# Kernel tuning notes

Measured on AMD Instinct MI355X. Metric: run time of the kernel, lower is better.

## Reference

```python
import jax, jax.numpy as jnp
import numpy as np

DT_MIN = 0.001  # config.rsp_dt_min
HARMONIC_SCALE = 0.1


def phi(z):
    # ResonantActivation: SiLU plus small harmonic term (harmonic_scale=0.1)
    return jax.nn.silu(z) + HARMONIC_SCALE * jnp.sin(z)


def setup_inputs() -> dict:
    key = jax.random.key(0)
    ks = jax.random.split(key, 8)
    B, L, D = 4, 2048, 1024
    std = 1.0 / np.sqrt(D)
    inp = {
        "x": jax.random.normal(ks[0], (B, L, D), dtype=jnp.float32),
        "f_prev": jnp.zeros((B, D), dtype=jnp.float32),
        "s_prev": jnp.zeros((B, D), dtype=jnp.float32),
        "w_lambda": jnp.zeros((D,), dtype=jnp.float32),
        "P_lambda_w": jax.random.uniform(ks[1], (D, D), jnp.float32, -std, std),
        "W_beta_w": jax.random.uniform(ks[2], (D, D), jnp.float32, -std, std),
        "W_alpha_w": jax.random.uniform(ks[3], (D, D), jnp.float32, -std, std),
        "W_alpha_b": jnp.full((D,), -3.0, dtype=jnp.float32),  # rsp_init_bias_alpha
        "W_rho_w": 0.01 * jax.random.normal(ks[4], (D, 3 * D), dtype=jnp.float32),
        "W_rho_b": jnp.full((D,), 2.0, dtype=jnp.float32),  # rsp_init_bias_rho
        "out_proj_w": 0.02 * jax.random.normal(ks[5], (D, D), dtype=jnp.float32),
        "res_scale": jnp.ones((1,), dtype=jnp.float32),
    }
    return inp


def _rsp_forward(x, f_prev, s_prev, w_lambda, P_lambda_w, W_beta_w,
                 W_alpha_w, W_alpha_b, W_rho_w, W_rho_b, out_proj_w, res_scale):
    # x: [B, L, D]
    # Input-dependent decay: lambda = exp(-exp(clip(w + x @ P^T)))
    lnl = jnp.clip(w_lambda + jnp.einsum('bld,ed->ble', x, P_lambda_w), -4.0, 4.0)
    lam = jnp.clip(jnp.exp(-jnp.exp(lnl)), DT_MIN, 1.0 - DT_MIN)

    B_gate = phi(jnp.einsum('bld,ed->ble', x, W_beta_w))
    alpha = jax.nn.sigmoid(jnp.einsum('bld,ed->ble', x, W_alpha_w) + W_alpha_b)

    # inject f_prev into first step's input contribution
    b_in = B_gate.at[:, 0, :].set(lam[:, 0, :] * f_prev + B_gate[:, 0, :])

    # fast linear recurrence: h_t = lam_t * h_{t-1} + b_t   (scan over L)
    lam_t = jnp.moveaxis(lam, 1, 0)      # [L, B, D]
    b_t = jnp.moveaxis(b_in, 1, 0)       # [L, B, D]

    def fast_step(h, lb):
        l, b = lb
        h = l * h + b
        return h, h

    _, f_seq = jax.lax.scan(fast_step, jnp.zeros_like(f_prev), (lam_t, b_t))
    f_states = jnp.moveaxis(f_seq, 0, 1)  # [B, L, D]

    # slow EMA: s_t = s_{t-1} + alpha_t * (f_t - s_{t-1})
    a_t = jnp.moveaxis(alpha, 1, 0)

    def slow_step(s, af):
        a, f = af
        s = s + a * (f - s)
        return s, s

    _, s_seq = jax.lax.scan(slow_step, s_prev, (a_t, f_seq))
    s_states = jnp.moveaxis(s_seq, 0, 1)  # [B, L, D]

    gate_input = jnp.concatenate([f_states, s_states, x], axis=-1)  # [B, L, 3D]
    rho = jax.nn.sigmoid(jnp.einsum('blk,ek->ble', gate_input, W_rho_w) + W_rho_b)
    h = rho * f_states + (1.0 - rho) * s_states
    h = x + res_scale * jnp.einsum('bld,ed->ble', h, out_proj_w)
    return h, f_states[:, -1, :], s_states[:, -1, :]


def reference(x, f_prev, s_prev, w_lambda, P_lambda_w, W_beta_w, W_alpha_w,
              W_alpha_b, W_rho_w, W_rho_b, out_proj_w, res_scale):
    return _rsp_forward(x, f_prev, s_prev, w_lambda, P_lambda_w, W_beta_w,
                        W_alpha_w, W_alpha_b, W_rho_w, W_rho_b, out_proj_w, res_scale)
```

## Files before the change

### kernel.cpp

```cpp
#include <hip/hip_runtime.h>

#define Bb 4
#define Ll 2048
#define Dd 1024
#define Mm (Bb*Ll)
#define NCH 64
#define CLEN (Ll/NCH)

typedef __attribute__((ext_vector_type(4))) float f32x4;
typedef __attribute__((ext_vector_type(8))) short s16x8;
typedef __attribute__((ext_vector_type(4))) short s16x4;

#define WAITV4 asm volatile("s_waitcnt vmcnt(4)" ::: "memory")
#define WAITV0 asm volatile("s_waitcnt vmcnt(0)" ::: "memory")
#define BARRAW asm volatile("s_barrier" ::: "memory")

__device__ __forceinline__ float sigm(float v){ return 1.0f/(1.0f+__expf(-v)); }

__device__ __forceinline__ short bf16rne(float f){
  unsigned u = __builtin_bit_cast(unsigned, f);
  u += 0x7fffu + ((u>>16)&1u);
  return (short)(u>>16);
}
__device__ __forceinline__ float bf2f(short s){
  unsigned u = ((unsigned)(unsigned short)s) << 16;
  return __builtin_bit_cast(float, u);
}

__device__ __forceinline__ void gl_lds16(const void* g, void* l){
  __builtin_amdgcn_global_load_lds((__attribute__((address_space(1))) void*)g,
                                   (__attribute__((address_space(3))) void*)l, 16, 0, 0);
}

template<int EPI>
__launch_bounds__(256)
__global__ void gemm_bt(const short* __restrict__ A0, const short* __restrict__ A1,
                        const short* __restrict__ A2, const short* __restrict__ W,
                        int K,
                        const float* __restrict__ b0, const float* __restrict__ b1,
                        const float* __restrict__ xres, const float* __restrict__ rsp,
                        const short* __restrict__ fB, const short* __restrict__ sB,
                        float* __restrict__ oF, unsigned short* __restrict__ oU,
                        short* __restrict__ oB0, short* __restrict__ oB1)
{
  __shared__ short As[3][128*32];
  __shared__ short Bs[3][128*32];
  const int tid  = threadIdx.x;
  const int lane = tid & 63;
  const int wid  = tid >> 6;
  const int wm = wid >> 1, wn = wid & 1;
  const long bn0 = (long)blockIdx.x * 128;
  const long bm0 = (long)blockIdx.y * 128;

  f32x4 acc[4][4] = {};

  const int r0 = tid >> 2;
  const int r1 = 64 + r0;
  const int j  = tid & 3;
  const int sw0 = (j ^ ((r0 >> 1) & 3)) * 8;
  const int sw1 = (j ^ ((r1 >> 1) & 3)) * 8;

  auto stage = [&](int buf, int k0){
    const short* Asrc = A0; long acol = k0;
    if (EPI == 3) {
      const int blk = k0 >> 10;
      Asrc = (blk == 0) ? A0 : ((blk == 1) ? A1 : A2);
      acol = k0 & 1023;
    }
    gl_lds16(Asrc + (bm0 + r0)*1024 + acol + sw0, &As[buf][(size_t)tid*8]);
    gl_lds16(Asrc + (bm0 + r1)*1024 + acol + sw1, &As[buf][(size_t)(256+tid)*8]);
    gl_lds16(W + (bn0 + r0)*(long)K + k0 + sw0, &Bs[buf][(size_t)tid*8]);
    gl_lds16(W + (bn0 + r1)*(long)K + k0 + sw1, &Bs[buf][(size_t)(256+tid)*8]);
  };

  auto compute = [&](int buf){
    const int q = lane >> 4;
    s16x8 af[4], bfr[4];
    #pragma unroll
    for (int mi = 0; mi < 4; ++mi) {
      const int row = wm*64 + mi*16 + (lane & 15);
      af[mi] = *(const s16x8*)&As[buf][row*32 + ((q ^ ((row>>1)&3)) << 3)];
    }
    #pragma unroll
    for (int ni = 0; ni < 4; ++ni) {
      const int row = wn*64 + ni*16 + (lane & 15);
      bfr[ni] = *(const s16x8*)&Bs[buf][row*32 + ((q ^ ((row>>1)&3)) << 3)];
    }
    #pragma unroll
    for (int mi = 0; mi < 4; ++mi)
      #pragma unroll
      for (int ni = 0; ni < 4; ++ni)
        asm("v_mfma_f32_16x16x32_bf16 %0, %1, %2, %0"
            : "+v"(acc[mi][ni]) : "v"(af[mi]), "v"(bfr[ni]));
  };

  const int NK = K >> 5;
  stage(0, 0);
  stage(1, 32);
  WAITV4;
  BARRAW;
  for (int it = 0; it < NK; ++it) {
    const bool pf = (it + 2) < NK;
    if (pf) stage((it + 2) % 3, (it + 2) << 5);
    compute(it % 3);
    if (pf) { WAITV4; } else { WAITV0; }
    BARRAW;
  }

  const float rs = (EPI == 4) ? rsp[0] : 0.0f;
  const int seg = (EPI == 5) ? (int)(bn0 >> 10) : 0;
  const int ecol0 = (int)bn0 + wn*64 + (lane & 15);
  const int erow0 = (int)bm0 + wm*64 + ((lane >> 4) << 2);

  #pragma unroll
  for (int mi = 0; mi < 4; ++mi) {
    #pragma unroll
    for (int ni = 0; ni < 4; ++ni) {
      asm volatile("s_nop 7\n\ts_nop 7\n\ts_nop 7" : "+v"(acc[mi][ni]));
      const f32x4 v = acc[mi][ni];
      const int gn = ecol0 + ni*16;
      const int cn = gn & 1023;
      #pragma unroll
      for (int jj = 0; jj < 4; ++jj) {
        const long gm  = erow0 + mi*16 + jj;
        const long idx = gm*1024 + cn;
        const float val = v[jj];
        if (EPI == 5) {
          if (seg == 0) {
            float z = val + b0[cn];
            z = fminf(fmaxf(z, -4.0f), 4.0f);
            float l = __expf(-__expf(z));
            l = fminf(fmaxf(l, 0.001f), 0.999f);
            oU[idx] = (unsigned short)__float2uint_rn(l * 65535.0f);
          } else if (seg == 1) {
            oB0[idx] = bf16rne(val*sigm(val) + 0.1f*__sinf(val));
          } else {
            oB1[idx] = bf16rne(sigm(val + b1[cn]));
          }
        } else if (EPI == 3) {
          const float r = sigm(val + b0[cn]);
          const float f = bf2f(fB[idx]);
          const float s = bf2f(sB[idx]);
          oB0[idx] = bf16rne(r*f + (1.0f - r)*s);
        } else {
          oF[idx] = xres[idx] + rs*val;
        }
      }
    }
  }
}


__global__ void f_chunk1(const unsigned short* __restrict__ lmU, const short* __restrict__ bgB,
                         const float* __restrict__ fprev,
                         float* __restrict__ cP, float* __restrict__ cB)
{
  const int d = blockIdx.x*256 + threadIdx.x;
  const int c = blockIdx.y, b = blockIdx.z;
  float P = 1.0f, Bv = 0.0f;
  size_t base = ((size_t)b*Ll + (size_t)c*CLEN)*Dd + d;
  const float fp = (c == 0) ? fprev[b*Dd + d] : 0.0f;
  for (int t = 0; t < CLEN; ++t) {
    const float l = (float)lmU[base] * (1.0f/65535.0f);
    float bb = bf2f(bgB[base]);
    if (c == 0 && t == 0) bb += l*fp;
    P *= l;
    Bv = l*Bv + bb;
    base += Dd;
  }
  const size_t ci = ((size_t)b*NCH + c)*Dd + d;
  cP[ci] = P; cB[ci] = Bv;
}

__global__ void scan_carry(const float* __restrict__ cP, const float* __restrict__ cB,
                           const float* __restrict__ init,
                           float* __restrict__ H0, float* __restrict__ last_out)
{
  const int d = blockIdx.x*256 + threadIdx.x;
  const int b = blockIdx.y;
  float h = init ? init[b*Dd + d] : 0.0f;
  for (int c = 0; c < NCH; ++c) {
    const size_t ci = ((size_t)b*NCH + c)*Dd + d;
    H0[ci] = h;
    h = cP[ci]*h + cB[ci];
  }
  last_out[b*Dd + d] = h;
}

__global__ void fs_mid(const unsigned short* __restrict__ lmU, const short* __restrict__ bgB,
                       const float* __restrict__ fprev, const float* __restrict__ H0f,
                       const short* __restrict__ alB,
                       short* __restrict__ fob, float* __restrict__ cPs,
                       float* __restrict__ cBs)
{
  const int d = blockIdx.x*256 + threadIdx.x;
  const int c = blockIdx.y, b = blockIdx.z;
  float h = H0f[((size_t)b*NCH + c)*Dd + d];
  float sP = 1.0f, sBv = 0.0f;
  size_t base = ((size_t)b*Ll + (size_t)c*CLEN)*Dd + d;
  const float fp = (c == 0) ? fprev[b*Dd + d] : 0.0f;
  for (int t = 0; t < CLEN; ++t) {
    const float l = (float)lmU[base] * (1.0f/65535.0f);
    float bb = bf2f(bgB[base]);
    if (c == 0 && t == 0) bb += l*fp;
    h = l*h + bb;
    const short hr = bf16rne(h);
    fob[base] = hr;
    const float fr = bf2f(hr);
    const float a = bf2f(alB[base]);
    sP *= (1.0f - a);
    sBv = (1.0f - a)*sBv + a*fr;
    base += Dd;
  }
  const size_t ci = ((size_t)b*NCH + c)*Dd + d;
  cPs[ci] = sP; cBs[ci] = sBv;
}

__global__ void s_chunk3(const short* __restrict__ alB, const short* __restrict__ fob,
                         const float* __restrict__ H0s, short* __restrict__ sob)
{
  const int d = blockIdx.x*256 + threadIdx.x;
  const int c = blockIdx.y, b = blockIdx.z;
  float h = H0s[((size_t)b*NCH + c)*Dd + d];
  size_t base = ((size_t)b*Ll + (size_t)c*CLEN)*Dd + d;
  for (int t = 0; t < CLEN; ++t) {
    const float a = bf2f(alB[base]);
    const float f = bf2f(fob[base]);
    h = h + a*(f - h);
    sob[base] = bf16rne(h);
    base += Dd;
  }
}

__global__ void cvt6(const float* __restrict__ a0, const float* __restrict__ a1,
                     const float* __restrict__ a2, const float* __restrict__ a3,
                     const float* __restrict__ a4, const float* __restrict__ a5,
                     short* __restrict__ dst)
{
  const int n0 = (Mm*Dd)/4, n1 = (Dd*Dd)/4, n4 = (3*Dd*Dd)/4;
  const int c1 = n0, c2 = c1+n1, c3 = c2+n1, c4 = c3+n1, c5 = c4+n4, total = c5+n1;
  int i = blockIdx.x*256 + threadIdx.x;
  for (; i < total; i += gridDim.x*256) {
    const float* src; int off;
    if      (i < c1) { src = a0; off = i; }
    else if (i < c2) { src = a1; off = i - c1; }
    else if (i < c3) { src = a2; off = i - c2; }
    else if (i < c4) { src = a3; off = i - c3; }
    else if (i < c5) { src = a4; off = i - c4; }
    else             { src = a5; off = i - c5; }
    const f32x4 v = ((const f32x4*)src)[off];
    s16x4 o;
    o[0] = bf16rne(v[0]); o[1] = bf16rne(v[1]);
    o[2] = bf16rne(v[2]); o[3] = bf16rne(v[3]);
    ((s16x4*)dst)[i] = o;
  }
}

extern "C" void kernel_launch(void* const* d_in, const int* in_sizes, int n_in,
                              void* d_out, int out_size, void* d_ws, size_t ws_size,
                              hipStream_t stream)
{
  (void)in_sizes; (void)n_in; (void)out_size; (void)ws_size;
  const float* x   = (const float*)d_in[0];
  const float* fpv = (const float*)d_in[1];
  const float* spv = (const float*)d_in[2];
  const float* wl  = (const float*)d_in[3];
  const float* Pw  = (const float*)d_in[4];
  const float* Wbw = (const float*)d_in[5];
  const float* Waw = (const float*)d_in[6];
  const float* ab  = (const float*)d_in[7];
  const float* Wr  = (const float*)d_in[8];
  const float* rb  = (const float*)d_in[9];
  const float* Wo  = (const float*)d_in[10];
  const float* rs  = (const float*)d_in[11];

  float* out    = (float*)d_out;
  float* f_last = out + (size_t)Mm*Dd;
  float* s_last = f_last + (size_t)Bb*Dd;

  char* w = (char*)d_ws;
  auto alloc = [&](size_t bytes){ char* p = w; w += (bytes + 255) & ~(size_t)255; return p; };
  short* xb   = (short*)alloc((size_t)Mm*Dd*2);
  short* w3   = (short*)alloc((size_t)3*Dd*Dd*2);
  short* wrb  = (short*)alloc((size_t)Dd*3*Dd*2);
  short* opb  = (short*)alloc((size_t)Dd*Dd*2);
  unsigned short* lamU = (unsigned short*)alloc((size_t)Mm*Dd*2);
  short* bgB  = (short*)alloc((size_t)Mm*Dd*2);
  short* alB  = (short*)alloc((size_t)Mm*Dd*2);
  short* fb   = (short*)alloc((size_t)Mm*Dd*2);
  short* sb   = (short*)alloc((size_t)Mm*Dd*2);
  float* cP   = (float*)alloc((size_t)Bb*NCH*Dd*4);
  float* cB   = (float*)alloc((size_t)Bb*NCH*Dd*4);
  float* H0   = (float*)alloc((size_t)Bb*NCH*Dd*4);
  short* hm   = (short*)lamU;

  cvt6<<<dim3(2048), dim3(256), 0, stream>>>(x, Pw, Wbw, Waw, Wr, Wo, xb);

  gemm_bt<5><<<dim3(3*Dd/128, Mm/128), dim3(256), 0, stream>>>(
      xb, nullptr, nullptr, w3, Dd, wl, ab, nullptr, nullptr, nullptr, nullptr,
      nullptr, lamU, bgB, alB);

  const dim3 gs(Dd/256, NCH, Bb);
  const dim3 gc(Dd/256, Bb);
  f_chunk1<<<gs, dim3(256), 0, stream>>>(lamU, bgB, fpv, cP, cB);
  scan_carry<<<gc, dim3(256), 0, stream>>>(cP, cB, (const float*)nullptr, H0, f_last);
  fs_mid<<<gs, dim3(256), 0, stream>>>(lamU, bgB, fpv, H0, alB, fb, cP, cB);
  scan_carry<<<gc, dim3(256), 0, stream>>>(cP, cB, spv, H0, s_last);
  s_chunk3<<<gs, dim3(256), 0, stream>>>(alB, fb, H0, sb);

  gemm_bt<3><<<dim3(Dd/128, Mm/128), dim3(256), 0, stream>>>(
      fb, sb, xb, wrb, 3*Dd, rb, nullptr, nullptr, nullptr, fb, sb,
      nullptr, nullptr, hm, nullptr);

  gemm_bt<4><<<dim3(Dd/128, Mm/128), dim3(256), 0, stream>>>(
      hm, nullptr, nullptr, opb, Dd, nullptr, nullptr, x, rs, nullptr, nullptr,
      out, nullptr, nullptr, nullptr);
}
```

Before: 366.4 us.

## Enlarge GEMM tiles to 256x128 with 512 threads and XCD-aware block remap

Switches the bf16 GEMM kernel from 128x128 tiles with 4 waves to 256x128 tiles with 8 waves, so each block stages twice as many A rows per B tile and reuses B more. It also launches a 1D grid and remaps block ids in groups of eight, in the style of AMD's XCD-aware ordering, so that neighbouring tiles land on the same die and share L2. The load count per stage falls from 4 to 3, so the vmcnt waits change to match. Risks are higher LDS use (about 72KB per block), which lowers occupancy, and fewer blocks per GEMM, which could leave CUs idle.

```diff
diff --git a/kernel.cpp b/kernel.cpp
--- a/kernel.cpp
+++ b/kernel.cpp
@@ -11,7 +11,7 @@
 typedef __attribute__((ext_vector_type(8))) short s16x8;
 typedef __attribute__((ext_vector_type(4))) short s16x4;
 
-#define WAITV4 asm volatile("s_waitcnt vmcnt(4)" ::: "memory")
+#define WAITV3 asm volatile("s_waitcnt vmcnt(3)" ::: "memory")
 #define WAITV0 asm volatile("s_waitcnt vmcnt(0)" ::: "memory")
 #define BARRAW asm volatile("s_barrier" ::: "memory")
 
@@ -32,8 +32,8 @@
                                    (__attribute__((address_space(3))) void*)l, 16, 0, 0);
 }
 
-template<int EPI>
-__launch_bounds__(256)
+template<int EPI, int NBX>
+__launch_bounds__(512)
 __global__ void gemm_bt(const short* __restrict__ A0, const short* __restrict__ A1,
                         const short* __restrict__ A2, const short* __restrict__ W,
                         int K,
@@ -43,22 +43,25 @@
                         float* __restrict__ oF, unsigned short* __restrict__ oU,
                         short* __restrict__ oB0, short* __restrict__ oB1)
 {
-  __shared__ short As[3][128*32];
+  __shared__ short As[3][256*32];
   __shared__ short Bs[3][128*32];
   const int tid  = threadIdx.x;
   const int lane = tid & 63;
   const int wid  = tid >> 6;
-  const int wm = wid >> 1, wn = wid & 1;
-  const long bn0 = (long)blockIdx.x * 128;
-  const long bm0 = (long)blockIdx.y * 128;
+  const int wm = wid >> 1;
+  const int wn = wid & 1;
+
+  const int cpx  = (int)gridDim.x >> 3;
+  const int wgid = ((int)blockIdx.x & 7) * cpx + ((int)blockIdx.x >> 3);
+  const long bn0 = (long)(wgid % NBX) * 128;
+  const long bm0 = (long)(wgid / NBX) * 256;
 
   f32x4 acc[4][4] = {};
 
   const int r0 = tid >> 2;
-  const int r1 = 64 + r0;
+  const int r1 = 128 + r0;
   const int j  = tid & 3;
-  const int sw0 = (j ^ ((r0 >> 1) & 3)) * 8;
-  const int sw1 = (j ^ ((r1 >> 1) & 3)) * 8;
+  const int sw = (j ^ ((r0 >> 1) & 3)) * 8;
 
   auto stage = [&](int buf, int k0){
     const short* Asrc = A0; long acol = k0;
@@ -67,10 +70,9 @@
       Asrc = (blk == 0) ? A0 : ((blk == 1) ? A1 : A2);
       acol = k0 & 1023;
     }
-    gl_lds16(Asrc + (bm0 + r0)*1024 + acol + sw0, &As[buf][(size_t)tid*8]);
-    gl_lds16(Asrc + (bm0 + r1)*1024 + acol + sw1, &As[buf][(size_t)(256+tid)*8]);
-    gl_lds16(W + (bn0 + r0)*(long)K + k0 + sw0, &Bs[buf][(size_t)tid*8]);
-    gl_lds16(W + (bn0 + r1)*(long)K + k0 + sw1, &Bs[buf][(size_t)(256+tid)*8]);
+    gl_lds16(Asrc + (bm0 + r0)*1024 + acol + sw, &As[buf][(size_t)tid*8]);
+    gl_lds16(Asrc + (bm0 + r1)*1024 + acol + sw, &As[buf][(size_t)(512+tid)*8]);
+    gl_lds16(W + (bn0 + r0)*(long)K + k0 + sw, &Bs[buf][(size_t)tid*8]);
   };
 
   auto compute = [&](int buf){
@@ -97,13 +99,13 @@
   const int NK = K >> 5;
   stage(0, 0);
   stage(1, 32);
-  WAITV4;
+  WAITV3;
   BARRAW;
   for (int it = 0; it < NK; ++it) {
     const bool pf = (it + 2) < NK;
     if (pf) stage((it + 2) % 3, (it + 2) << 5);
     compute(it % 3);
-    if (pf) { WAITV4; } else { WAITV0; }
+    if (pf) { WAITV3; } else { WAITV0; }
     BARRAW;
   }
 
@@ -296,7 +298,7 @@
 
   cvt6<<<dim3(2048), dim3(256), 0, stream>>>(x, Pw, Wbw, Waw, Wr, Wo, xb);
 
-  gemm_bt<5><<<dim3(3*Dd/128, Mm/128), dim3(256), 0, stream>>>(
+  gemm_bt<5, 24><<<dim3(768), dim3(512), 0, stream>>>(
       xb, nullptr, nullptr, w3, Dd, wl, ab, nullptr, nullptr, nullptr, nullptr,
       nullptr, lamU, bgB, alB);
 
@@ -308,11 +310,11 @@
   scan_carry<<<gc, dim3(256), 0, stream>>>(cP, cB, spv, H0, s_last);
   s_chunk3<<<gs, dim3(256), 0, stream>>>(alB, fb, H0, sb);
 
-  gemm_bt<3><<<dim3(Dd/128, Mm/128), dim3(256), 0, stream>>>(
+  gemm_bt<3, 8><<<dim3(256), dim3(512), 0, stream>>>(
       fb, sb, xb, wrb, 3*Dd, rb, nullptr, nullptr, nullptr, fb, sb,
       nullptr, nullptr, hm, nullptr);
 
-  gemm_bt<4><<<dim3(Dd/128, Mm/128), dim3(256), 0, stream>>>(
+  gemm_bt<4, 8><<<dim3(256), dim3(512), 0, stream>>>(
       hm, nullptr, nullptr, opb, Dd, nullptr, nullptr, x, rs, nullptr, nullptr,
       out, nullptr, nullptr, nullptr);
 }
```

Result: slower. 391.5 us (+6.9%).

## Deepen GEMM LDS pipeline to five stages and remap workgroups per XCD

Applied to the files above, without the earlier changes.

The bf16 GEMM kernel goes from a 3-buffer to a 5-buffer LDS ring, staging four K-tiles ahead with graded vmcnt waits. This is meant to hide more global-load latency. Launches switch to a 1D grid whose block index is remapped so consecutive tiles share an XCD, aiming for better L2 reuse across the 8 XCDs. LDS use rises from 48KB to 80KB per block, which may lower occupancy.

```diff
diff --git a/kernel.cpp b/kernel.cpp
--- a/kernel.cpp
+++ b/kernel.cpp
@@ -11,9 +11,11 @@
 typedef __attribute__((ext_vector_type(8))) short s16x8;
 typedef __attribute__((ext_vector_type(4))) short s16x4;
 
-#define WAITV4 asm volatile("s_waitcnt vmcnt(4)" ::: "memory")
-#define WAITV0 asm volatile("s_waitcnt vmcnt(0)" ::: "memory")
-#define BARRAW asm volatile("s_barrier" ::: "memory")
+#define WAITV12 asm volatile("s_waitcnt vmcnt(12)" ::: "memory")
+#define WAITV8  asm volatile("s_waitcnt vmcnt(8)"  ::: "memory")
+#define WAITV4  asm volatile("s_waitcnt vmcnt(4)"  ::: "memory")
+#define WAITV0  asm volatile("s_waitcnt vmcnt(0)"  ::: "memory")
+#define BARRAW  asm volatile("s_barrier" ::: "memory")
 
 __device__ __forceinline__ float sigm(float v){ return 1.0f/(1.0f+__expf(-v)); }
 
@@ -32,7 +34,7 @@
                                    (__attribute__((address_space(3))) void*)l, 16, 0, 0);
 }
 
-template<int EPI>
+template<int EPI, int NBX>
 __launch_bounds__(256)
 __global__ void gemm_bt(const short* __restrict__ A0, const short* __restrict__ A1,
                         const short* __restrict__ A2, const short* __restrict__ W,
@@ -43,14 +45,17 @@
                         float* __restrict__ oF, unsigned short* __restrict__ oU,
                         short* __restrict__ oB0, short* __restrict__ oB1)
 {
-  __shared__ short As[3][128*32];
-  __shared__ short Bs[3][128*32];
+  __shared__ short As[5*128*32];
+  __shared__ short Bs[5*128*32];
   const int tid  = threadIdx.x;
   const int lane = tid & 63;
   const int wid  = tid >> 6;
   const int wm = wid >> 1, wn = wid & 1;
-  const long bn0 = (long)blockIdx.x * 128;
-  const long bm0 = (long)blockIdx.y * 128;
+
+  const int cpx  = (int)gridDim.x >> 3;
+  const int wgid = ((int)blockIdx.x & 7) * cpx + ((int)blockIdx.x >> 3);
+  const long bn0 = (long)(wgid % NBX) * 128;
+  const long bm0 = (long)(wgid / NBX) * 128;
 
   f32x4 acc[4][4] = {};
 
@@ -67,24 +72,28 @@
       Asrc = (blk == 0) ? A0 : ((blk == 1) ? A1 : A2);
       acol = k0 & 1023;
     }
-    gl_lds16(Asrc + (bm0 + r0)*1024 + acol + sw0, &As[buf][(size_t)tid*8]);
-    gl_lds16(Asrc + (bm0 + r1)*1024 + acol + sw1, &As[buf][(size_t)(256+tid)*8]);
-    gl_lds16(W + (bn0 + r0)*(long)K + k0 + sw0, &Bs[buf][(size_t)tid*8]);
-    gl_lds16(W + (bn0 + r1)*(long)K + k0 + sw1, &Bs[buf][(size_t)(256+tid)*8]);
+    short* ab = As + buf*4096;
+    short* bb = Bs + buf*4096;
+    gl_lds16(Asrc + (bm0 + r0)*1024 + acol + sw0, ab + (size_t)tid*8);
+    gl_lds16(Asrc + (bm0 + r1)*1024 + acol + sw1, ab + (size_t)(256+tid)*8);
+    gl_lds16(W + (bn0 + r0)*(long)K + k0 + sw0, bb + (size_t)tid*8);
+    gl_lds16(W + (bn0 + r1)*(long)K + k0 + sw1, bb + (size_t)(256+tid)*8);
   };
 
   auto compute = [&](int buf){
     const int q = lane >> 4;
+    const short* ab = As + buf*4096;
+    const short* bb = Bs + buf*4096;
     s16x8 af[4], bfr[4];
     #pragma unroll
     for (int mi = 0; mi < 4; ++mi) {
       const int row = wm*64 + mi*16 + (lane & 15);
-      af[mi] = *(const s16x8*)&As[buf][row*32 + ((q ^ ((row>>1)&3)) << 3)];
+      af[mi] = *(const s16x8*)&ab[row*32 + ((q ^ ((row>>1)&3)) << 3)];
     }
     #pragma unroll
     for (int ni = 0; ni < 4; ++ni) {
       const int row = wn*64 + ni*16 + (lane & 15);
-      bfr[ni] = *(const s16x8*)&Bs[buf][row*32 + ((q ^ ((row>>1)&3)) << 3)];
+      bfr[ni] = *(const s16x8*)&bb[row*32 + ((q ^ ((row>>1)&3)) << 3)];
     }
     #pragma unroll
     for (int mi = 0; mi < 4; ++mi)
@@ -95,16 +104,21 @@
   };
 
   const int NK = K >> 5;
-  stage(0, 0);
-  stage(1, 32);
-  WAITV4;
+  stage(0, 0); stage(1, 32); stage(2, 64); stage(3, 96);
+  WAITV12;
   BARRAW;
+  int cur = 0, nxt = 4;
   for (int it = 0; it < NK; ++it) {
-    const bool pf = (it + 2) < NK;
-    if (pf) stage((it + 2) % 3, (it + 2) << 5);
-    compute(it % 3);
-    if (pf) { WAITV4; } else { WAITV0; }
+    if (it + 4 < NK) stage(nxt, (it + 4) << 5);
+    compute(cur);
+    const int ahead = ((it + 4 < NK) ? (it + 4) : (NK - 1)) - (it + 1);
+    if (ahead >= 3)      { WAITV12; }
+    else if (ahead == 2) { WAITV8; }
+    else if (ahead == 1) { WAITV4; }
+    else                 { WAITV0; }
     BARRAW;
+    if (++cur == 5) cur = 0;
+    if (++nxt == 5) nxt = 0;
   }
 
   const float rs = (EPI == 4) ? rsp[0] : 0.0f;
@@ -296,7 +310,7 @@
 
   cvt6<<<dim3(2048), dim3(256), 0, stream>>>(x, Pw, Wbw, Waw, Wr, Wo, xb);
 
-  gemm_bt<5><<<dim3(3*Dd/128, Mm/128), dim3(256), 0, stream>>>(
+  gemm_bt<5, 24><<<dim3(1536), dim3(256), 0, stream>>>(
       xb, nullptr, nullptr, w3, Dd, wl, ab, nullptr, nullptr, nullptr, nullptr,
       nullptr, lamU, bgB, alB);
 
@@ -308,11 +322,11 @@
   scan_carry<<<gc, dim3(256), 0, stream>>>(cP, cB, spv, H0, s_last);
   s_chunk3<<<gs, dim3(256), 0, stream>>>(alB, fb, H0, sb);
 
-  gemm_bt<3><<<dim3(Dd/128, Mm/128), dim3(256), 0, stream>>>(
+  gemm_bt<3, 8><<<dim3(512), dim3(256), 0, stream>>>(
       fb, sb, xb, wrb, 3*Dd, rb, nullptr, nullptr, nullptr, fb, sb,
       nullptr, nullptr, hm, nullptr);
 
-  gemm_bt<4><<<dim3(Dd/128, Mm/128), dim3(256), 0, stream>>>(
+  gemm_bt<4, 8><<<dim3(512), dim3(256), 0, stream>>>(
       hm, nullptr, nullptr, opb, Dd, nullptr, nullptr, x, rs, nullptr, nullptr,
       out, nullptr, nullptr, nullptr);
 }
```

Result: slower. 389.0 us (+6.2%).
